# Optimization experiments

Hardware: AMD Instinct MI355X
Metric: run time of the kernel (lower is better)

The kernel has to match this reference:

```python
import jax, jax.numpy as jnp
import numpy as np


def setup_inputs() -> dict:
    key = jax.random.key(0)
    ks = jax.random.split(key, 10)
    B, T = 64, 2048
    inp_p, inp_q, out = 512, 512, 512
    def xavier(k, shape):
        fan_in, fan_out = shape[1], shape[0]
        limit = np.sqrt(6.0 / (fan_in + fan_out))
        return jax.random.uniform(k, shape, jnp.float32, -limit, limit)
    return {
        "input_p": jax.random.normal(ks[0], (B, inp_p), jnp.float32),
        "input_q": jax.random.normal(ks[1], (B, T, inp_q), jnp.float32),
        "h_tm1": jax.random.normal(ks[2], (B, out), jnp.float32),
        "Wp": xavier(ks[3], (out, inp_p)),
        "bp": jnp.zeros((out,), jnp.float32),
        "Wq": xavier(ks[4], (out, inp_q)),
        "bq": jnp.zeros((out,), jnp.float32),
        "Wr": xavier(ks[5], (out, out)),
        "br": jnp.zeros((out,), jnp.float32),
        "w": 0.05 * jax.random.normal(ks[6], (out,), jnp.float32),
        "match_b": jnp.ones((1,), jnp.float32),
        "depth": 0,
    }


def reference(input_p, input_q, h_tm1, Wp, bp, Wq, bq, Wr, br, w, match_b, depth):
    # depth selects the layer; single layer (depth=0) parameters provided.
    G_p = (input_p @ Wp.T + bp)[:, None, :]          # [B, 1, out]
    G_q = jnp.einsum("btq,oq->bto", input_q, Wq) + bq  # [B, T, out]
    G_r = (h_tm1 @ Wr.T + br)[:, None, :]            # [B, 1, out]
    G = jnp.tanh(G_p + G_q + G_r)                    # [B, T, out]
    alpha = jnp.einsum("bto,o->bt", G, w) + match_b[0]  # [B, T]
    alpha = jax.nn.softmax(alpha, axis=-1)
    z = jnp.einsum("bt,btq->bq", alpha, input_q)     # [B, inp_q]
    return jnp.concatenate([input_p, z], axis=1)     # [B, inp_p+inp_q]
```

## Files before the change

kernel.cpp:

```cpp
#include <hip/hip_runtime.h>
#include <hip/hip_bf16.h>
#include <stdint.h>
#include <stddef.h>


typedef __attribute__((ext_vector_type(8))) short short8;
typedef __attribute__((ext_vector_type(8))) unsigned short ushort8v;
typedef __attribute__((ext_vector_type(4))) float f32x4;

__device__ __forceinline__ unsigned short f2bf(float f) {
    unsigned int u = __builtin_bit_cast(unsigned int, f);
    return (unsigned short)((u + 0x7FFFu + ((u >> 16) & 1u)) >> 16);
}

__device__ __forceinline__ uint2 cvt4(float4 a) {
    union { __hip_bfloat162 h[2]; uint2 v; } u;
    u.h[0] = __float22bfloat162_rn(make_float2(a.x, a.y));
    u.h[1] = __float22bfloat162_rn(make_float2(a.z, a.w));
    return u.v;
}

__device__ __forceinline__ float bf2f(unsigned short u) {
    unsigned v = (unsigned)u << 16;
    return __builtin_bit_cast(float, v);
}

__device__ __forceinline__ void gload_lds16(const void* g, void* l) {
    __builtin_amdgcn_global_load_lds(
        (const __attribute__((address_space(1))) unsigned int*)g,
        (__attribute__((address_space(3))) unsigned int*)l, 16, 0, 0);
}

__global__ __launch_bounds__(256) void k_convert8(const float* __restrict__ src,
                                                  unsigned short* __restrict__ dst) {
    size_t i = ((size_t)blockIdx.x * 256 + threadIdx.x) * 8;
    float4 a = *(const float4*)(src + i);
    float4 b = *(const float4*)(src + i + 4);
    uint2 lo = cvt4(a), hi = cvt4(b);
    union { uint2 u[2]; short8 s; } p;
    p.u[0] = lo; p.u[1] = hi;
    *(short8*)(dst + i) = p.s;
}

__global__ __launch_bounds__(256) void k_prq(
        const float* __restrict__ ip, const float* __restrict__ h,
        const float* __restrict__ Wp, const float* __restrict__ Wr,
        const float* __restrict__ bp, const float* __restrict__ bq,
        const float* __restrict__ br, float* __restrict__ prq) {
    __shared__ float ip_lds[64][68];
    __shared__ float h_lds[64][68];
    __shared__ float wp_lds[8][68];
    __shared__ float wr_lds[8][68];
    const int tid = threadIdx.x;
    const int o0 = blockIdx.x * 8;
    const int bb = tid >> 3;
    const int oo = tid & 7;
    float acc0 = 0.f, acc1 = 0.f;
    const int lrow = tid >> 2;
    const int lcol = (tid & 3) * 16;
    for (int kc = 0; kc < 512; kc += 64) {
        #pragma unroll
        for (int j = 0; j < 16; j += 4) {
            float4 v = *(const float4*)(ip + lrow * 512 + kc + lcol + j);
            ip_lds[lrow][lcol + j] = v.x; ip_lds[lrow][lcol + j + 1] = v.y;
            ip_lds[lrow][lcol + j + 2] = v.z; ip_lds[lrow][lcol + j + 3] = v.w;
            float4 u = *(const float4*)(h + lrow * 512 + kc + lcol + j);
            h_lds[lrow][lcol + j] = u.x; h_lds[lrow][lcol + j + 1] = u.y;
            h_lds[lrow][lcol + j + 2] = u.z; h_lds[lrow][lcol + j + 3] = u.w;
        }
        if (tid < 128) {
            int r = tid >> 4, c = (tid & 15) * 4;
            float4 v = *(const float4*)(Wp + (size_t)(o0 + r) * 512 + kc + c);
            wp_lds[r][c] = v.x; wp_lds[r][c + 1] = v.y; wp_lds[r][c + 2] = v.z; wp_lds[r][c + 3] = v.w;
        } else {
            int t2 = tid - 128;
            int r = t2 >> 4, c = (t2 & 15) * 4;
            float4 v = *(const float4*)(Wr + (size_t)(o0 + r) * 512 + kc + c);
            wr_lds[r][c] = v.x; wr_lds[r][c + 1] = v.y; wr_lds[r][c + 2] = v.z; wr_lds[r][c + 3] = v.w;
        }
        __syncthreads();
        #pragma unroll 4
        for (int k = 0; k < 64; ++k) {
            float wpv = wp_lds[oo][k], wrv = wr_lds[oo][k];
            acc0 += ip_lds[bb][k] * wpv + h_lds[bb][k] * wrv;
            acc1 += ip_lds[bb + 32][k] * wpv + h_lds[bb + 32][k] * wrv;
        }
        __syncthreads();
    }
    const int o = o0 + oo;
    float base = bp[o] + bq[o] + br[o];
    prq[bb * 512 + o] = acc0 + base;
    prq[(bb + 32) * 512 + o] = acc1 + base;
}

union ZB { unsigned short B[2][16384]; float zp[8][512]; };

__global__ __launch_bounds__(512, 2) void k_fused(
        const float* __restrict__ iq, const unsigned short* __restrict__ Wq_bf,
        const float* __restrict__ prq, const float* __restrict__ wv,
        float* __restrict__ zp_g, float* __restrict__ ms_g) {
    __shared__ unsigned short A_p[16][2064];
    __shared__ ZB sB;
    __shared__ float w_lds[512];
    __shared__ float prq_lds[512];
    __shared__ float red[4][64];
    __shared__ float e_lds[64];

    const int tid = threadIdx.x;
    const int bid = blockIdx.x;
    const int m0 = bid * 64;
    const int b = bid >> 5;

    w_lds[tid] = wv[tid];
    prq_lds[tid] = prq[b * 512 + tid];

    const int lane = tid & 63;
    const int wave = tid >> 6;
    const int wm = wave >> 2;
    const int wn = wave & 3;
    const int r16 = lane & 15;
    const int cc = lane >> 4;
    const int swz = ((cc ^ ((r16 >> 1) & 3)) << 3);

    const int arow = tid >> 3;
    const int afg = tid & 7;
    const float* asrc = iq + (size_t)(m0 + arow) * 512 + afg * 4;
    const int adst_off = arow * 32 + ((((afg >> 1)) ^ ((arow >> 1) & 3)) << 3) + (afg & 1) * 4;

    const unsigned short *bsrc0, *bsrc1, *bsrc2, *bsrc3;
    {
        int c0 = tid,        r0 = c0 >> 2, s0 = (c0 & 3) ^ ((r0 >> 1) & 3);
        int c1 = 512 + tid,  r1 = c1 >> 2, s1 = (c1 & 3) ^ ((r1 >> 1) & 3);
        int c2 = 1024 + tid, r2 = c2 >> 2, s2 = (c2 & 3) ^ ((r2 >> 1) & 3);
        int c3 = 1536 + tid, r3 = c3 >> 2, s3 = (c3 & 3) ^ ((r3 >> 1) & 3);
        bsrc0 = Wq_bf + (size_t)r0 * 512 + (s0 << 3);
        bsrc1 = Wq_bf + (size_t)r1 * 512 + (s1 << 3);
        bsrc2 = Wq_bf + (size_t)r2 * 512 + (s2 << 3);
        bsrc3 = Wq_bf + (size_t)r3 * 512 + (s3 << 3);
    }

#define BSTAGE(KT, BUF)                                                             \
    gload_lds16(bsrc0 + (KT) * 32, (char*)&sB.B[BUF][0] + 0 * 8192 + wave * 1024);  \
    gload_lds16(bsrc1 + (KT) * 32, (char*)&sB.B[BUF][0] + 1 * 8192 + wave * 1024);  \
    gload_lds16(bsrc2 + (KT) * 32, (char*)&sB.B[BUF][0] + 2 * 8192 + wave * 1024);  \
    gload_lds16(bsrc3 + (KT) * 32, (char*)&sB.B[BUF][0] + 3 * 8192 + wave * 1024);

    f32x4 acc[2][8];
    #pragma unroll
    for (int i = 0; i < 2; ++i)
        #pragma unroll
        for (int j = 0; j < 8; ++j) acc[i][j] = (f32x4){0.f, 0.f, 0.f, 0.f};

    float4 raA, raB;

    raA = *(const float4*)(asrc);
    BSTAGE(0, 0);
    asm volatile("s_waitcnt vmcnt(4)" ::: "memory");
    *(uint2*)&A_p[0][adst_off] = cvt4(raA);
    asm volatile("s_waitcnt lgkmcnt(0)" ::: "memory");
    __builtin_amdgcn_s_barrier();
    raA = *(const float4*)(asrc + 32);
    BSTAGE(1, 1);
    asm volatile("s_waitcnt vmcnt(5)" ::: "memory");
    __builtin_amdgcn_s_barrier();

#define ITER(KT, RC, RN)                                                                  \
    {                                                                                     \
        const unsigned short* Ab = &A_p[KT][0];                                           \
        const unsigned short* Bb = &sB.B[(KT) & 1][0];                                    \
        short8 af0 = *(const short8*)&Ab[(wm * 32 + r16) * 32 + swz];                     \
        short8 af1 = *(const short8*)&Ab[(wm * 32 + 16 + r16) * 32 + swz];                \
        _Pragma("unroll")                                                                 \
        for (int nf = 0; nf < 8; ++nf) {                                                  \
            short8 bfr = *(const short8*)&Bb[(wn * 128 + nf * 16 + r16) * 32 + swz];      \
            acc[0][nf] = __builtin_amdgcn_mfma_f32_16x16x32_bf16(af0, bfr, acc[0][nf], 0, 0, 0); \
            acc[1][nf] = __builtin_amdgcn_mfma_f32_16x16x32_bf16(af1, bfr, acc[1][nf], 0, 0, 0); \
        }                                                                                 \
        if ((KT) < 15) {                                                                  \
            asm volatile("s_waitcnt vmcnt(4)" ::: "memory");     \
            *(uint2*)&A_p[(KT) + 1][adst_off] = cvt4(RC);                                 \
            asm volatile("s_waitcnt lgkmcnt(0)" ::: "memory");                            \
            __builtin_amdgcn_s_barrier();       \
            if ((KT) < 14) {                                                              \
                RN = *(const float4*)(asrc + ((KT) + 2) * 32);                            \
                BSTAGE((KT) + 2, (KT) & 1);                                               \
                asm volatile("s_waitcnt vmcnt(5)" ::: "memory");      \
            } else {                                                                      \
                asm volatile("s_waitcnt vmcnt(0)" ::: "memory");                          \
            }                                                                             \
            __builtin_amdgcn_s_barrier();                                                 \
        }                                                                                 \
    }

    for (int kt = 0; kt < 16; kt += 2) {
        ITER(kt, raA, raB);
        ITER(kt + 1, raB, raA);
    }
#undef ITER
#undef BSTAGE

    float part[2][4];
    #pragma unroll
    for (int mf = 0; mf < 2; ++mf)
        #pragma unroll
        for (int j = 0; j < 4; ++j) part[mf][j] = 0.f;

    #pragma unroll
    for (int nf = 0; nf < 8; ++nf) {
        int c = wn * 128 + nf * 16 + r16;
        float wc = w_lds[c];
        float pc = prq_lds[c];
        #pragma unroll
        for (int mf = 0; mf < 2; ++mf) {
            #pragma unroll
            for (int j = 0; j < 4; ++j) {
                float x = acc[mf][nf][j] + pc;
                float e = __expf(2.f * x);
                part[mf][j] += wc * (1.f - 2.f / (e + 1.f));
            }
        }
    }
    #pragma unroll
    for (int mf = 0; mf < 2; ++mf)
        #pragma unroll
        for (int j = 0; j < 4; ++j) {
            float v = part[mf][j];
            v += __shfl_xor(v, 1);
            v += __shfl_xor(v, 2);
            v += __shfl_xor(v, 4);
            v += __shfl_xor(v, 8);
            part[mf][j] = v;
        }
    if (r16 == 0) {
        #pragma unroll
        for (int mf = 0; mf < 2; ++mf)
            #pragma unroll
            for (int j = 0; j < 4; ++j)
                red[wn][wm * 32 + mf * 16 + cc * 4 + j] = part[mf][j];
    }
    __syncthreads();

    if (tid < 64) {
        float l = red[0][tid] + red[1][tid] + red[2][tid] + red[3][tid];
        float m = l;
        #pragma unroll
        for (int d = 1; d < 64; d <<= 1) m = fmaxf(m, __shfl_xor(m, d));
        float ev = __expf(l - m);
        float s = ev;
        #pragma unroll
        for (int d = 1; d < 64; d <<= 1) s += __shfl_xor(s, d);
        e_lds[tid] = ev;
        if (tid == 0) { ms_g[bid * 2] = m; ms_g[bid * 2 + 1] = s; }
    }
    __syncthreads();

    const int q0 = (tid & 63) * 8;
    const int kt_q = q0 >> 5;
    const int ec = (q0 >> 3) & 3;
    float zq[8];
    #pragma unroll
    for (int k = 0; k < 8; ++k) zq[k] = 0.f;
    #pragma unroll
    for (int ti = 0; ti < 8; ++ti) {
        int t = (tid >> 6) * 8 + ti;
        float ev = e_lds[t];
        short8 av = *(const short8*)&A_p[kt_q][t * 32 + ((ec ^ ((t >> 1) & 3)) << 3)];
        #pragma unroll
        for (int k = 0; k < 8; ++k) zq[k] += ev * bf2f((unsigned short)av[k]);
    }
    __syncthreads();
    float* zrow = &sB.zp[tid >> 6][0];
    *(float4*)&zrow[q0]     = make_float4(zq[0], zq[1], zq[2], zq[3]);
    *(float4*)&zrow[q0 + 4] = make_float4(zq[4], zq[5], zq[6], zq[7]);
    __syncthreads();
    float z = 0.f;
    #pragma unroll
    for (int w = 0; w < 8; ++w) z += sB.zp[w][tid];
    zp_g[(size_t)bid * 512 + tid] = z;
}

__global__ __launch_bounds__(512) void k_comb(const float* __restrict__ zp,
                                              const float* __restrict__ ms,
                                              const float* __restrict__ ip,
                                              float* __restrict__ out) {
    const int b = blockIdx.x, tid = threadIdx.x;
    __shared__ float mm[32], ssv[32];
    if (tid < 32) {
        mm[tid] = ms[(b * 32 + tid) * 2];
        ssv[tid] = ms[(b * 32 + tid) * 2 + 1];
    }
    __syncthreads();
    float M = -1e30f;
    #pragma unroll
    for (int i = 0; i < 32; ++i) M = fmaxf(M, mm[i]);
    float S = 0.f, z = 0.f;
    #pragma unroll 4
    for (int i = 0; i < 32; ++i) {
        float sc = __expf(mm[i] - M);
        S += ssv[i] * sc;
        z += sc * zp[(size_t)(b * 32 + i) * 512 + tid];
    }
    out[b * 1024 + 512 + tid] = z / S;
    out[b * 1024 + tid] = ip[b * 512 + tid];
}

extern "C" void kernel_launch(void* const* d_in, const int* in_sizes, int n_in,
                              void* d_out, int out_size, void* d_ws, size_t ws_size,
                              hipStream_t stream) {
    const float* input_p = (const float*)d_in[0];
    const float* input_q = (const float*)d_in[1];
    const float* h_tm1   = (const float*)d_in[2];
    const float* Wp      = (const float*)d_in[3];
    const float* bp      = (const float*)d_in[4];
    const float* Wq      = (const float*)d_in[5];
    const float* bq      = (const float*)d_in[6];
    const float* Wr      = (const float*)d_in[7];
    const float* br      = (const float*)d_in[8];
    const float* wv      = (const float*)d_in[9];
    float* out = (float*)d_out;

    char* ws = (char*)d_ws;
    unsigned short* Wq_bf = (unsigned short*)ws;
    float* prq  = (float*)(ws + 512 * 1024);
    float* ms   = (float*)(ws + 640 * 1024);
    float* zp   = (float*)(ws + 1024 * 1024);

    k_convert8<<<dim3(128), dim3(256), 0, stream>>>(Wq, Wq_bf);
    k_prq<<<dim3(64), dim3(256), 0, stream>>>(input_p, h_tm1, Wp, Wr, bp, bq, br, prq);
    k_fused<<<dim3(2048), dim3(512), 0, stream>>>(input_q, Wq_bf, prq, wv, zp, ms);
    k_comb<<<dim3(64), dim3(512), 0, stream>>>(zp, ms, input_p, out);
}
```

Before: 224.3 us.

## Stage full 128-row input tile in LDS and read Wq directly from global

```diff
diff --git a/kernel.cpp b/kernel.cpp
--- a/kernel.cpp
+++ b/kernel.cpp
@@ -5,30 +5,20 @@
 
 
 typedef __attribute__((ext_vector_type(8))) short short8;
-typedef __attribute__((ext_vector_type(8))) unsigned short ushort8v;
 typedef __attribute__((ext_vector_type(4))) float f32x4;
 
-__device__ __forceinline__ unsigned short f2bf(float f) {
-    unsigned int u = __builtin_bit_cast(unsigned int, f);
-    return (unsigned short)((u + 0x7FFFu + ((u >> 16) & 1u)) >> 16);
-}
-
-__device__ __forceinline__ uint2 cvt4(float4 a) {
-    union { __hip_bfloat162 h[2]; uint2 v; } u;
+__device__ __forceinline__ short8 cvt8(float4 a, float4 b) {
+    union { __hip_bfloat162 h[4]; short8 s; } u;
     u.h[0] = __float22bfloat162_rn(make_float2(a.x, a.y));
     u.h[1] = __float22bfloat162_rn(make_float2(a.z, a.w));
-    return u.v;
+    u.h[2] = __float22bfloat162_rn(make_float2(b.x, b.y));
+    u.h[3] = __float22bfloat162_rn(make_float2(b.z, b.w));
+    return u.s;
 }
 
 __device__ __forceinline__ float bf2f(unsigned short u) {
     unsigned v = (unsigned)u << 16;
     return __builtin_bit_cast(float, v);
-}
-
-__device__ __forceinline__ void gload_lds16(const void* g, void* l) {
-    __builtin_amdgcn_global_load_lds(
-        (const __attribute__((address_space(1))) unsigned int*)g,
-        (__attribute__((address_space(3))) unsigned int*)l, 16, 0, 0);
 }
 
 __global__ __launch_bounds__(256) void k_convert8(const float* __restrict__ src,
@@ -36,10 +26,7 @@
     size_t i = ((size_t)blockIdx.x * 256 + threadIdx.x) * 8;
     float4 a = *(const float4*)(src + i);
     float4 b = *(const float4*)(src + i + 4);
-    uint2 lo = cvt4(a), hi = cvt4(b);
-    union { uint2 u[2]; short8 s; } p;
-    p.u[0] = lo; p.u[1] = hi;
-    *(short8*)(dst + i) = p.s;
+    *(short8*)(dst + i) = cvt8(a, b);
 }
 
 __global__ __launch_bounds__(256) void k_prq(
@@ -93,26 +80,37 @@
     prq[(bb + 32) * 512 + o] = acc1 + base;
 }
 
-union ZB { unsigned short B[2][16384]; float zp[8][512]; };
-
-__global__ __launch_bounds__(512, 2) void k_fused(
+__global__ __launch_bounds__(512, 1) void k_big(
         const float* __restrict__ iq, const unsigned short* __restrict__ Wq_bf,
         const float* __restrict__ prq, const float* __restrict__ wv,
         float* __restrict__ zp_g, float* __restrict__ ms_g) {
-    __shared__ unsigned short A_p[16][2064];
-    __shared__ ZB sB;
+    __shared__ unsigned short A_p[128 * 512];
     __shared__ float w_lds[512];
     __shared__ float prq_lds[512];
-    __shared__ float red[4][64];
-    __shared__ float e_lds[64];
+    __shared__ float red[4][128];
+    __shared__ float e_lds[128];
+    __shared__ float zsc[8][512];
 
     const int tid = threadIdx.x;
     const int bid = blockIdx.x;
-    const int m0 = bid * 64;
-    const int b = bid >> 5;
+    const int m0 = bid * 128;
+    const int b = bid >> 4;
 
     w_lds[tid] = wv[tid];
     prq_lds[tid] = prq[b * 512 + tid];
+
+    {
+        const int srow = tid >> 2;
+        const float* gbase = iq + (size_t)(m0 + srow) * 512;
+        #pragma unroll 4
+        for (int r = 0; r < 16; ++r) {
+            int c = (tid & 3) + r * 4;
+            float4 v0 = *(const float4*)(gbase + c * 8);
+            float4 v1 = *(const float4*)(gbase + c * 8 + 4);
+            *(short8*)&A_p[srow * 512 + ((c ^ (srow & 7)) << 3)] = cvt8(v0, v1);
+        }
+    }
+    __syncthreads();
 
     const int lane = tid & 63;
     const int wave = tid >> 6;
@@ -120,88 +118,40 @@
     const int wn = wave & 3;
     const int r16 = lane & 15;
     const int cc = lane >> 4;
-    const int swz = ((cc ^ ((r16 >> 1) & 3)) << 3);
-
-    const int arow = tid >> 3;
-    const int afg = tid & 7;
-    const float* asrc = iq + (size_t)(m0 + arow) * 512 + afg * 4;
-    const int adst_off = arow * 32 + ((((afg >> 1)) ^ ((arow >> 1) & 3)) << 3) + (afg & 1) * 4;
-
-    const unsigned short *bsrc0, *bsrc1, *bsrc2, *bsrc3;
-    {
-        int c0 = tid,        r0 = c0 >> 2, s0 = (c0 & 3) ^ ((r0 >> 1) & 3);
-        int c1 = 512 + tid,  r1 = c1 >> 2, s1 = (c1 & 3) ^ ((r1 >> 1) & 3);
-        int c2 = 1024 + tid, r2 = c2 >> 2, s2 = (c2 & 3) ^ ((r2 >> 1) & 3);
-        int c3 = 1536 + tid, r3 = c3 >> 2, s3 = (c3 & 3) ^ ((r3 >> 1) & 3);
-        bsrc0 = Wq_bf + (size_t)r0 * 512 + (s0 << 3);
-        bsrc1 = Wq_bf + (size_t)r1 * 512 + (s1 << 3);
-        bsrc2 = Wq_bf + (size_t)r2 * 512 + (s2 << 3);
-        bsrc3 = Wq_bf + (size_t)r3 * 512 + (s3 << 3);
-    }
-
-#define BSTAGE(KT, BUF)                                                             \
-    gload_lds16(bsrc0 + (KT) * 32, (char*)&sB.B[BUF][0] + 0 * 8192 + wave * 1024);  \
-    gload_lds16(bsrc1 + (KT) * 32, (char*)&sB.B[BUF][0] + 1 * 8192 + wave * 1024);  \
-    gload_lds16(bsrc2 + (KT) * 32, (char*)&sB.B[BUF][0] + 2 * 8192 + wave * 1024);  \
-    gload_lds16(bsrc3 + (KT) * 32, (char*)&sB.B[BUF][0] + 3 * 8192 + wave * 1024);
-
-    f32x4 acc[2][8];
-    #pragma unroll
-    for (int i = 0; i < 2; ++i)
+    const int xr = r16 & 7;
+
+    f32x4 acc[4][8];
+    #pragma unroll
+    for (int i = 0; i < 4; ++i)
         #pragma unroll
         for (int j = 0; j < 8; ++j) acc[i][j] = (f32x4){0.f, 0.f, 0.f, 0.f};
 
-    float4 raA, raB;
-
-    raA = *(const float4*)(asrc);
-    BSTAGE(0, 0);
-    asm volatile("s_waitcnt vmcnt(4)" ::: "memory");
-    *(uint2*)&A_p[0][adst_off] = cvt4(raA);
-    asm volatile("s_waitcnt lgkmcnt(0)" ::: "memory");
-    __builtin_amdgcn_s_barrier();
-    raA = *(const float4*)(asrc + 32);
-    BSTAGE(1, 1);
-    asm volatile("s_waitcnt vmcnt(5)" ::: "memory");
-    __builtin_amdgcn_s_barrier();
-
-#define ITER(KT, RC, RN)                                                                  \
-    {                                                                                     \
-        const unsigned short* Ab = &A_p[KT][0];                                           \
-        const unsigned short* Bb = &sB.B[(KT) & 1][0];                                    \
-        short8 af0 = *(const short8*)&Ab[(wm * 32 + r16) * 32 + swz];                     \
-        short8 af1 = *(const short8*)&Ab[(wm * 32 + 16 + r16) * 32 + swz];                \
-        _Pragma("unroll")                                                                 \
-        for (int nf = 0; nf < 8; ++nf) {                                                  \
-            short8 bfr = *(const short8*)&Bb[(wn * 128 + nf * 16 + r16) * 32 + swz];      \
-            acc[0][nf] = __builtin_amdgcn_mfma_f32_16x16x32_bf16(af0, bfr, acc[0][nf], 0, 0, 0); \
-            acc[1][nf] = __builtin_amdgcn_mfma_f32_16x16x32_bf16(af1, bfr, acc[1][nf], 0, 0, 0); \
-        }                                                                                 \
-        if ((KT) < 15) {                                                                  \
-            asm volatile("s_waitcnt vmcnt(4)" ::: "memory");     \
-            *(uint2*)&A_p[(KT) + 1][adst_off] = cvt4(RC);                                 \
-            asm volatile("s_waitcnt lgkmcnt(0)" ::: "memory");                            \
-            __builtin_amdgcn_s_barrier();       \
-            if ((KT) < 14) {                                                              \
-                RN = *(const float4*)(asrc + ((KT) + 2) * 32);                            \
-                BSTAGE((KT) + 2, (KT) & 1);                                               \
-                asm volatile("s_waitcnt vmcnt(5)" ::: "memory");      \
-            } else {                                                                      \
-                asm volatile("s_waitcnt vmcnt(0)" ::: "memory");                          \
-            }                                                                             \
-            __builtin_amdgcn_s_barrier();                                                 \
-        }                                                                                 \
-    }
-
-    for (int kt = 0; kt < 16; kt += 2) {
-        ITER(kt, raA, raB);
-        ITER(kt + 1, raB, raA);
-    }
-#undef ITER
-#undef BSTAGE
-
-    float part[2][4];
-    #pragma unroll
-    for (int mf = 0; mf < 2; ++mf)
+    const unsigned short* bbase = Wq_bf + ((size_t)(wn * 128 + r16)) * 512 + cc * 8;
+    const int arow0 = (wm * 64 + r16) * 512;
+
+    #pragma unroll 2
+    for (int kc = 0; kc < 16; ++kc) {
+        short8 bf[8];
+        #pragma unroll
+        for (int nf = 0; nf < 8; ++nf)
+            bf[nf] = *(const short8*)(bbase + (size_t)nf * 16 * 512 + kc * 32);
+        short8 af[4];
+        #pragma unroll
+        for (int mf = 0; mf < 4; ++mf) {
+            int c = kc * 4 + cc;
+            af[mf] = *(const short8*)&A_p[arow0 + mf * 16 * 512 + (((c ^ xr)) << 3)];
+        }
+        #pragma unroll
+        for (int nf = 0; nf < 8; ++nf) {
+            #pragma unroll
+            for (int mf = 0; mf < 4; ++mf)
+                acc[mf][nf] = __builtin_amdgcn_mfma_f32_16x16x32_bf16(af[mf], bf[nf], acc[mf][nf], 0, 0, 0);
+        }
+    }
+
+    float part[4][4];
+    #pragma unroll
+    for (int mf = 0; mf < 4; ++mf)
         #pragma unroll
         for (int j = 0; j < 4; ++j) part[mf][j] = 0.f;
 
@@ -211,7 +161,7 @@
         float wc = w_lds[c];
         float pc = prq_lds[c];
         #pragma unroll
-        for (int mf = 0; mf < 2; ++mf) {
+        for (int mf = 0; mf < 4; ++mf) {
             #pragma unroll
             for (int j = 0; j < 4; ++j) {
                 float x = acc[mf][nf][j] + pc;
@@ -221,7 +171,7 @@
         }
     }
     #pragma unroll
-    for (int mf = 0; mf < 2; ++mf)
+    for (int mf = 0; mf < 4; ++mf)
         #pragma unroll
         for (int j = 0; j < 4; ++j) {
             float v = part[mf][j];
@@ -233,50 +183,55 @@
         }
     if (r16 == 0) {
         #pragma unroll
-        for (int mf = 0; mf < 2; ++mf)
+        for (int mf = 0; mf < 4; ++mf)
             #pragma unroll
             for (int j = 0; j < 4; ++j)
-                red[wn][wm * 32 + mf * 16 + cc * 4 + j] = part[mf][j];
-    }
-    __syncthreads();
-
+                red[wn][wm * 64 + mf * 16 + cc * 4 + j] = part[mf][j];
+    }
+    __syncthreads();
+
+    if (tid < 128)
+        e_lds[tid] = red[0][tid] + red[1][tid] + red[2][tid] + red[3][tid];
+    __syncthreads();
     if (tid < 64) {
-        float l = red[0][tid] + red[1][tid] + red[2][tid] + red[3][tid];
-        float m = l;
+        float l0 = e_lds[tid], l1 = e_lds[tid + 64];
+        float m = fmaxf(l0, l1);
         #pragma unroll
         for (int d = 1; d < 64; d <<= 1) m = fmaxf(m, __shfl_xor(m, d));
-        float ev = __expf(l - m);
-        float s = ev;
+        float e0 = __expf(l0 - m), e1 = __expf(l1 - m);
+        float s = e0 + e1;
         #pragma unroll
         for (int d = 1; d < 64; d <<= 1) s += __shfl_xor(s, d);
-        e_lds[tid] = ev;
+        e_lds[tid] = e0;
+        e_lds[tid + 64] = e1;
         if (tid == 0) { ms_g[bid * 2] = m; ms_g[bid * 2 + 1] = s; }
     }
     __syncthreads();
 
-    const int q0 = (tid & 63) * 8;
-    const int kt_q = q0 >> 5;
-    const int ec = (q0 >> 3) & 3;
-    float zq[8];
-    #pragma unroll
-    for (int k = 0; k < 8; ++k) zq[k] = 0.f;
-    #pragma unroll
-    for (int ti = 0; ti < 8; ++ti) {
-        int t = (tid >> 6) * 8 + ti;
-        float ev = e_lds[t];
-        short8 av = *(const short8*)&A_p[kt_q][t * 32 + ((ec ^ ((t >> 1) & 3)) << 3)];
-        #pragma unroll
-        for (int k = 0; k < 8; ++k) zq[k] += ev * bf2f((unsigned short)av[k]);
-    }
-    __syncthreads();
-    float* zrow = &sB.zp[tid >> 6][0];
-    *(float4*)&zrow[q0]     = make_float4(zq[0], zq[1], zq[2], zq[3]);
-    *(float4*)&zrow[q0 + 4] = make_float4(zq[4], zq[5], zq[6], zq[7]);
-    __syncthreads();
-    float z = 0.f;
-    #pragma unroll
-    for (int w = 0; w < 8; ++w) z += sB.zp[w][tid];
-    zp_g[(size_t)bid * 512 + tid] = z;
+    {
+        const int c = tid & 63;
+        const int ts = tid >> 6;
+        float zq[8];
+        #pragma unroll
+        for (int k = 0; k < 8; ++k) zq[k] = 0.f;
+        #pragma unroll 4
+        for (int ti = 0; ti < 16; ++ti) {
+            int t = ts * 16 + ti;
+            float ev = e_lds[t];
+            short8 av = *(const short8*)&A_p[t * 512 + ((c ^ (t & 7)) << 3)];
+            #pragma unroll
+            for (int k = 0; k < 8; ++k) zq[k] += ev * bf2f((unsigned short)av[k]);
+        }
+        *(float4*)&zsc[ts][c * 8]     = make_float4(zq[0], zq[1], zq[2], zq[3]);
+        *(float4*)&zsc[ts][c * 8 + 4] = make_float4(zq[4], zq[5], zq[6], zq[7]);
+    }
+    __syncthreads();
+    {
+        float z = 0.f;
+        #pragma unroll
+        for (int w = 0; w < 8; ++w) z += zsc[w][tid];
+        zp_g[(size_t)bid * 512 + tid] = z;
+    }
 }
 
 __global__ __launch_bounds__(512) void k_comb(const float* __restrict__ zp,
@@ -284,21 +239,21 @@
                                               const float* __restrict__ ip,
                                               float* __restrict__ out) {
     const int b = blockIdx.x, tid = threadIdx.x;
-    __shared__ float mm[32], ssv[32];
-    if (tid < 32) {
-        mm[tid] = ms[(b * 32 + tid) * 2];
-        ssv[tid] = ms[(b * 32 + tid) * 2 + 1];
+    __shared__ float mm[16], ssv[16];
+    if (tid < 16) {
+        mm[tid] = ms[(b * 16 + tid) * 2];
+        ssv[tid] = ms[(b * 16 + tid) * 2 + 1];
     }
     __syncthreads();
     float M = -1e30f;
     #pragma unroll
-    for (int i = 0; i < 32; ++i) M = fmaxf(M, mm[i]);
+    for (int i = 0; i < 16; ++i) M = fmaxf(M, mm[i]);
     float S = 0.f, z = 0.f;
     #pragma unroll 4
-    for (int i = 0; i < 32; ++i) {
+    for (int i = 0; i < 16; ++i) {
         float sc = __expf(mm[i] - M);
         S += ssv[i] * sc;
-        z += sc * zp[(size_t)(b * 32 + i) * 512 + tid];
+        z += sc * zp[(size_t)(b * 16 + i) * 512 + tid];
     }
     out[b * 1024 + 512 + tid] = z / S;
     out[b * 1024 + tid] = ip[b * 512 + tid];
@@ -327,6 +282,6 @@
 
     k_convert8<<<dim3(128), dim3(256), 0, stream>>>(Wq, Wq_bf);
     k_prq<<<dim3(64), dim3(256), 0, stream>>>(input_p, h_tm1, Wp, Wr, bp, bq, br, prq);
-    k_fused<<<dim3(2048), dim3(512), 0, stream>>>(input_q, Wq_bf, prq, wv, zp, ms);
+    k_big<<<dim3(1024), dim3(512), 0, stream>>>(input_q, Wq_bf, prq, wv, zp, ms);
     k_comb<<<dim3(64), dim3(512), 0, stream>>>(zp, ms, input_p, out);
 }
```

New measurement: 230.3 us. +2.7%, slower.

## Use 1024-thread blocks with upfront A conversion and single-buffer-ahead B pipeline

Applied to the files above, without the earlier changes.

```diff
diff --git a/kernel.cpp b/kernel.cpp
--- a/kernel.cpp
+++ b/kernel.cpp
@@ -5,19 +5,15 @@
 
 
 typedef __attribute__((ext_vector_type(8))) short short8;
-typedef __attribute__((ext_vector_type(8))) unsigned short ushort8v;
 typedef __attribute__((ext_vector_type(4))) float f32x4;
 
-__device__ __forceinline__ unsigned short f2bf(float f) {
-    unsigned int u = __builtin_bit_cast(unsigned int, f);
-    return (unsigned short)((u + 0x7FFFu + ((u >> 16) & 1u)) >> 16);
-}
-
-__device__ __forceinline__ uint2 cvt4(float4 a) {
-    union { __hip_bfloat162 h[2]; uint2 v; } u;
+__device__ __forceinline__ short8 cvt8(float4 a, float4 b) {
+    union { __hip_bfloat162 h[4]; short8 s; } u;
     u.h[0] = __float22bfloat162_rn(make_float2(a.x, a.y));
     u.h[1] = __float22bfloat162_rn(make_float2(a.z, a.w));
-    return u.v;
+    u.h[2] = __float22bfloat162_rn(make_float2(b.x, b.y));
+    u.h[3] = __float22bfloat162_rn(make_float2(b.z, b.w));
+    return u.s;
 }
 
 __device__ __forceinline__ float bf2f(unsigned short u) {
@@ -36,10 +32,7 @@
     size_t i = ((size_t)blockIdx.x * 256 + threadIdx.x) * 8;
     float4 a = *(const float4*)(src + i);
     float4 b = *(const float4*)(src + i + 4);
-    uint2 lo = cvt4(a), hi = cvt4(b);
-    union { uint2 u[2]; short8 s; } p;
-    p.u[0] = lo; p.u[1] = hi;
-    *(short8*)(dst + i) = p.s;
+    *(short8*)(dst + i) = cvt8(a, b);
 }
 
 __global__ __launch_bounds__(256) void k_prq(
@@ -93,17 +86,17 @@
     prq[(bb + 32) * 512 + o] = acc1 + base;
 }
 
-union ZB { unsigned short B[2][16384]; float zp[8][512]; };
-
-__global__ __launch_bounds__(512, 2) void k_fused(
+union BZ { unsigned short B[2][16384]; float zsc[8][512]; };
+
+__global__ __launch_bounds__(1024, 4) void k_fused(
         const float* __restrict__ iq, const unsigned short* __restrict__ Wq_bf,
         const float* __restrict__ prq, const float* __restrict__ wv,
         float* __restrict__ zp_g, float* __restrict__ ms_g) {
     __shared__ unsigned short A_p[16][2064];
-    __shared__ ZB sB;
+    __shared__ BZ sh;
     __shared__ float w_lds[512];
     __shared__ float prq_lds[512];
-    __shared__ float red[4][64];
+    __shared__ float red[8][64];
     __shared__ float e_lds[64];
 
     const int tid = threadIdx.x;
@@ -111,92 +104,85 @@
     const int m0 = bid * 64;
     const int b = bid >> 5;
 
-    w_lds[tid] = wv[tid];
-    prq_lds[tid] = prq[b * 512 + tid];
+    if (tid < 512) {
+        w_lds[tid] = wv[tid];
+        prq_lds[tid] = prq[b * 512 + tid];
+    }
+
+    {
+        const int row = tid >> 4;
+        const float* g = iq + (size_t)(m0 + row) * 512;
+        #pragma unroll
+        for (int i = 0; i < 4; ++i) {
+            int gc = (tid & 15) + i * 16;
+            float4 v0 = *(const float4*)(g + gc * 8);
+            float4 v1 = *(const float4*)(g + gc * 8 + 4);
+            *(short8*)&A_p[gc >> 2][row * 32 + (((gc & 3) ^ ((row >> 1) & 3)) << 3)] = cvt8(v0, v1);
+        }
+    }
+
+    const unsigned short *bsrc0, *bsrc1;
+    {
+        int r0 = tid >> 2, s0 = (tid & 3) ^ ((r0 >> 1) & 3);
+        bsrc0 = Wq_bf + (size_t)r0 * 512 + (s0 << 3);
+        int t1 = 1024 + tid, r1 = t1 >> 2, s1 = (t1 & 3) ^ ((r1 >> 1) & 3);
+        bsrc1 = Wq_bf + (size_t)r1 * 512 + (s1 << 3);
+    }
+    const int wave = tid >> 6;
+
+#define BSTAGE(S, BUF)                                                               \
+    gload_lds16(bsrc0 + (S) * 32, (char*)&sh.B[BUF][0] + wave * 1024);               \
+    gload_lds16(bsrc1 + (S) * 32, (char*)&sh.B[BUF][0] + 16384 + wave * 1024);
+
+    BSTAGE(0, 0);
+    asm volatile("s_waitcnt vmcnt(0) lgkmcnt(0)" ::: "memory");
+    __builtin_amdgcn_sched_barrier(0);
+    __builtin_amdgcn_s_barrier();
 
     const int lane = tid & 63;
-    const int wave = tid >> 6;
-    const int wm = wave >> 2;
-    const int wn = wave & 3;
+    const int wm = wave >> 3;
+    const int ng = wave & 7;
     const int r16 = lane & 15;
     const int cc = lane >> 4;
-    const int swz = ((cc ^ ((r16 >> 1) & 3)) << 3);
-
-    const int arow = tid >> 3;
-    const int afg = tid & 7;
-    const float* asrc = iq + (size_t)(m0 + arow) * 512 + afg * 4;
-    const int adst_off = arow * 32 + ((((afg >> 1)) ^ ((arow >> 1) & 3)) << 3) + (afg & 1) * 4;
-
-    const unsigned short *bsrc0, *bsrc1, *bsrc2, *bsrc3;
-    {
-        int c0 = tid,        r0 = c0 >> 2, s0 = (c0 & 3) ^ ((r0 >> 1) & 3);
-        int c1 = 512 + tid,  r1 = c1 >> 2, s1 = (c1 & 3) ^ ((r1 >> 1) & 3);
-        int c2 = 1024 + tid, r2 = c2 >> 2, s2 = (c2 & 3) ^ ((r2 >> 1) & 3);
-        int c3 = 1536 + tid, r3 = c3 >> 2, s3 = (c3 & 3) ^ ((r3 >> 1) & 3);
-        bsrc0 = Wq_bf + (size_t)r0 * 512 + (s0 << 3);
-        bsrc1 = Wq_bf + (size_t)r1 * 512 + (s1 << 3);
-        bsrc2 = Wq_bf + (size_t)r2 * 512 + (s2 << 3);
-        bsrc3 = Wq_bf + (size_t)r3 * 512 + (s3 << 3);
-    }
-
-#define BSTAGE(KT, BUF)                                                             \
-    gload_lds16(bsrc0 + (KT) * 32, (char*)&sB.B[BUF][0] + 0 * 8192 + wave * 1024);  \
-    gload_lds16(bsrc1 + (KT) * 32, (char*)&sB.B[BUF][0] + 1 * 8192 + wave * 1024);  \
-    gload_lds16(bsrc2 + (KT) * 32, (char*)&sB.B[BUF][0] + 2 * 8192 + wave * 1024);  \
-    gload_lds16(bsrc3 + (KT) * 32, (char*)&sB.B[BUF][0] + 3 * 8192 + wave * 1024);
-
-    f32x4 acc[2][8];
+
+    const int ar0 = wm * 32 + r16;
+    const int ar1 = ar0 + 16;
+    const int aoff0 = ar0 * 32 + ((cc ^ ((ar0 >> 1) & 3)) << 3);
+    const int aoff1 = ar1 * 32 + ((cc ^ ((ar1 >> 1) & 3)) << 3);
+    int boff[4];
+    #pragma unroll
+    for (int nf = 0; nf < 4; ++nf) {
+        int brow = ng * 64 + nf * 16 + r16;
+        boff[nf] = brow * 32 + ((cc ^ ((brow >> 1) & 3)) << 3);
+    }
+
+    f32x4 acc[2][4];
     #pragma unroll
     for (int i = 0; i < 2; ++i)
         #pragma unroll
-        for (int j = 0; j < 8; ++j) acc[i][j] = (f32x4){0.f, 0.f, 0.f, 0.f};
-
-    float4 raA, raB;
-
-    raA = *(const float4*)(asrc);
-    BSTAGE(0, 0);
-    asm volatile("s_waitcnt vmcnt(4)" ::: "memory");
-    *(uint2*)&A_p[0][adst_off] = cvt4(raA);
-    asm volatile("s_waitcnt lgkmcnt(0)" ::: "memory");
-    __builtin_amdgcn_s_barrier();
-    raA = *(const float4*)(asrc + 32);
-    BSTAGE(1, 1);
-    asm volatile("s_waitcnt vmcnt(5)" ::: "memory");
-    __builtin_amdgcn_s_barrier();
-
-#define ITER(KT, RC, RN)                                                                  \
-    {                                                                                     \
-        const unsigned short* Ab = &A_p[KT][0];                                           \
-        const unsigned short* Bb = &sB.B[(KT) & 1][0];                                    \
-        short8 af0 = *(const short8*)&Ab[(wm * 32 + r16) * 32 + swz];                     \
-        short8 af1 = *(const short8*)&Ab[(wm * 32 + 16 + r16) * 32 + swz];                \
-        _Pragma("unroll")                                                                 \
-        for (int nf = 0; nf < 8; ++nf) {                                                  \
-            short8 bfr = *(const short8*)&Bb[(wn * 128 + nf * 16 + r16) * 32 + swz];      \
-            acc[0][nf] = __builtin_amdgcn_mfma_f32_16x16x32_bf16(af0, bfr, acc[0][nf], 0, 0, 0); \
-            acc[1][nf] = __builtin_amdgcn_mfma_f32_16x16x32_bf16(af1, bfr, acc[1][nf], 0, 0, 0); \
-        }                                                                                 \
-        if ((KT) < 15) {                                                                  \
-            asm volatile("s_waitcnt vmcnt(4)" ::: "memory");     \
-            *(uint2*)&A_p[(KT) + 1][adst_off] = cvt4(RC);                                 \
-            asm volatile("s_waitcnt lgkmcnt(0)" ::: "memory");                            \
-            __builtin_amdgcn_s_barrier();       \
-            if ((KT) < 14) {                                                              \
-                RN = *(const float4*)(asrc + ((KT) + 2) * 32);                            \
-                BSTAGE((KT) + 2, (KT) & 1);                                               \
-                asm volatile("s_waitcnt vmcnt(5)" ::: "memory");      \
-            } else {                                                                      \
-                asm volatile("s_waitcnt vmcnt(0)" ::: "memory");                          \
-            }                                                                             \
-            __builtin_amdgcn_s_barrier();                                                 \
-        }                                                                                 \
-    }
-
-    for (int kt = 0; kt < 16; kt += 2) {
-        ITER(kt, raA, raB);
-        ITER(kt + 1, raB, raA);
-    }
-#undef ITER
+        for (int j = 0; j < 4; ++j) acc[i][j] = (f32x4){0.f, 0.f, 0.f, 0.f};
+
+    #pragma unroll 2
+    for (int s = 0; s < 16; ++s) {
+        if (s < 15) {
+            BSTAGE(s + 1, (s + 1) & 1);
+            asm volatile("s_waitcnt vmcnt(2)" ::: "memory");
+        } else {
+            asm volatile("s_waitcnt vmcnt(0)" ::: "memory");
+        }
+        __builtin_amdgcn_s_barrier();
+        const unsigned short* Bb = &sh.B[s & 1][0];
+        short8 af0 = *(const short8*)&A_p[s][aoff0];
+        short8 af1 = *(const short8*)&A_p[s][aoff1];
+        #pragma unroll
+        for (int nf = 0; nf < 4; ++nf) {
+            short8 bfr = *(const short8*)&Bb[boff[nf]];
+            acc[0][nf] = __builtin_amdgcn_mfma_f32_16x16x32_bf16(af0, bfr, acc[0][nf], 0, 0, 0);
+            acc[1][nf] = __builtin_amdgcn_mfma_f32_16x16x32_bf16(af1, bfr, acc[1][nf], 0, 0, 0);
+        }
+        asm volatile("s_waitcnt lgkmcnt(0)" ::: "memory");
+        __builtin_amdgcn_s_barrier();
+    }
 #undef BSTAGE
 
     float part[2][4];
@@ -206,8 +192,8 @@
         for (int j = 0; j < 4; ++j) part[mf][j] = 0.f;
 
     #pragma unroll
-    for (int nf = 0; nf < 8; ++nf) {
-        int c = wn * 128 + nf * 16 + r16;
+    for (int nf = 0; nf < 4; ++nf) {
+        int c = ng * 64 + nf * 16 + r16;
         float wc = w_lds[c];
         float pc = prq_lds[c];
         #pragma unroll
@@ -236,47 +222,52 @@
         for (int mf = 0; mf < 2; ++mf)
             #pragma unroll
             for (int j = 0; j < 4; ++j)
-                red[wn][wm * 32 + mf * 16 + cc * 4 + j] = part[mf][j];
+                red[ng][wm * 32 + mf * 16 + cc * 4 + j] = part[mf][j];
     }
     __syncthreads();
 
     if (tid < 64) {
-        float l = red[0][tid] + red[1][tid] + red[2][tid] + red[3][tid];
+        float l = red[0][tid] + red[1][tid] + red[2][tid] + red[3][tid]
+                + red[4][tid] + red[5][tid] + red[6][tid] + red[7][tid];
         float m = l;
         #pragma unroll
         for (int d = 1; d < 64; d <<= 1) m = fmaxf(m, __shfl_xor(m, d));
         float ev = __expf(l - m);
-        float s = ev;
-        #pragma unroll
-        for (int d = 1; d < 64; d <<= 1) s += __shfl_xor(s, d);
+        float sv = ev;
+        #pragma unroll
+        for (int d = 1; d < 64; d <<= 1) sv += __shfl_xor(sv, d);
         e_lds[tid] = ev;
-        if (tid == 0) { ms_g[bid * 2] = m; ms_g[bid * 2 + 1] = s; }
+        if (tid == 0) { ms_g[bid * 2] = m; ms_g[bid * 2 + 1] = sv; }
     }
     __syncthreads();
 
-    const int q0 = (tid & 63) * 8;
-    const int kt_q = q0 >> 5;
-    const int ec = (q0 >> 3) & 3;
-    float zq[8];
-    #pragma unroll
-    for (int k = 0; k < 8; ++k) zq[k] = 0.f;
-    #pragma unroll
-    for (int ti = 0; ti < 8; ++ti) {
-        int t = (tid >> 6) * 8 + ti;
-        float ev = e_lds[t];
-        short8 av = *(const short8*)&A_p[kt_q][t * 32 + ((ec ^ ((t >> 1) & 3)) << 3)];
-        #pragma unroll
-        for (int k = 0; k < 8; ++k) zq[k] += ev * bf2f((unsigned short)av[k]);
+    {
+        const int qg = tid & 127;
+        const int tg = tid >> 7;
+        const int q0 = qg * 4;
+        const int sl = q0 >> 5;
+        const int qc = (q0 >> 3) & 3;
+        const int qo = q0 & 7;
+        float z0 = 0.f, z1 = 0.f, z2 = 0.f, z3 = 0.f;
+        #pragma unroll
+        for (int ti = 0; ti < 8; ++ti) {
+            int t = tg * 8 + ti;
+            float ev = e_lds[t];
+            const unsigned short* ap = &A_p[sl][t * 32 + ((qc ^ ((t >> 1) & 3)) << 3) + qo];
+            z0 += ev * bf2f(ap[0]);
+            z1 += ev * bf2f(ap[1]);
+            z2 += ev * bf2f(ap[2]);
+            z3 += ev * bf2f(ap[3]);
+        }
+        *(float4*)&sh.zsc[tg][q0] = make_float4(z0, z1, z2, z3);
     }
     __syncthreads();
-    float* zrow = &sB.zp[tid >> 6][0];
-    *(float4*)&zrow[q0]     = make_float4(zq[0], zq[1], zq[2], zq[3]);
-    *(float4*)&zrow[q0 + 4] = make_float4(zq[4], zq[5], zq[6], zq[7]);
-    __syncthreads();
-    float z = 0.f;
-    #pragma unroll
-    for (int w = 0; w < 8; ++w) z += sB.zp[w][tid];
-    zp_g[(size_t)bid * 512 + tid] = z;
+    if (tid < 512) {
+        float z = 0.f;
+        #pragma unroll
+        for (int w = 0; w < 8; ++w) z += sh.zsc[w][tid];
+        zp_g[(size_t)bid * 512 + tid] = z;
+    }
 }
 
 __global__ __launch_bounds__(512) void k_comb(const float* __restrict__ zp,
@@ -327,6 +318,6 @@
 
     k_convert8<<<dim3(128), dim3(256), 0, stream>>>(Wq, Wq_bf);
     k_prq<<<dim3(64), dim3(256), 0, stream>>>(input_p, h_tm1, Wp, Wr, bp, bq, br, prq);
-    k_fused<<<dim3(2048), dim3(512), 0, stream>>>(input_q, Wq_bf, prq, wv, zp, ms);
+    k_fused<<<dim3(2048), dim3(1024), 0, stream>>>(input_q, Wq_bf, prq, wv, zp, ms);
     k_comb<<<dim3(64), dim3(512), 0, stream>>>(zp, ms, input_p, out);
 }
```

Measured after the change: 218.6 us. 2.5% less time.
